# Kernel tuning notes

Measured on AMD Instinct MI355X. Metric: run time of the kernel, lower is better.

Reference implementation:

```python
import jax, jax.numpy as jnp
import numpy as np

N_NODES = 100000
N_EDGES = 1600000


def _degree_norms(src, dst, n):
    ones = jnp.ones(src.shape[0], dtype=jnp.float32)
    deg_out = jax.ops.segment_sum(ones, src, num_segments=n)
    deg_in = jax.ops.segment_sum(ones, dst, num_segments=n)
    src_norm = jax.lax.rsqrt(jnp.maximum(deg_out, 1.0))
    dst_norm = jax.lax.rsqrt(jnp.maximum(deg_in, 1.0))
    return src_norm, dst_norm


def _graph_conv(x, W, b, src, dst, src_norm, dst_norm, n):
    # DGL GraphConv, norm='both': D_dst^{-1/2} A D_src^{-1/2} X W + b
    # Apply W first (same math, smaller messages).
    h = x @ W                                  # [N, out]
    m = (h * src_norm[:, None])[src]           # [E, out] gather
    agg = jax.ops.segment_sum(m, dst, num_segments=n)  # [N, out] scatter-add
    return agg * dst_norm[:, None] + b


def setup_inputs() -> dict:
    key = jax.random.key(0)
    ks = jax.random.split(key, 10)
    inp = {
        "x": jax.random.normal(ks[0], (N_NODES, 128), dtype=jnp.float32),
        "src": jax.random.randint(ks[1], (N_EDGES,), 0, N_NODES, dtype=jnp.int32),
        "dst": jax.random.randint(ks[2], (N_EDGES,), 0, N_NODES, dtype=jnp.int32),
        "W1": jax.random.normal(ks[3], (128, 64), dtype=jnp.float32) * 0.08,
        "b1": jnp.zeros((64,), dtype=jnp.float32),
        "W2": jax.random.normal(ks[4], (64, 64), dtype=jnp.float32) * 0.12,
        "b2": jnp.zeros((64,), dtype=jnp.float32),
        "W3": jax.random.normal(ks[5], (64, 64), dtype=jnp.float32) * 0.12,
        "b3": jnp.zeros((64,), dtype=jnp.float32),
        "W4": jax.random.normal(ks[6], (64, 64), dtype=jnp.float32) * 0.12,
        "b4": jnp.zeros((64,), dtype=jnp.float32),
        "Wres": jax.random.normal(ks[7], (128, 64), dtype=jnp.float32) * 0.08,
        "bres": jnp.zeros((64,), dtype=jnp.float32),
        "Wop": jax.random.normal(ks[8], (64, 16), dtype=jnp.float32) * 0.12,
        "bop": jnp.zeros((16,), dtype=jnp.float32),
    }
    return inp


def reference(x, src, dst, W1, b1, W2, b2, W3, b3, W4, b4, Wres, bres, Wop, bop):
    n = x.shape[0]
    src_norm, dst_norm = _degree_norms(src, dst, n)
    res = x @ Wres + bres
    out = jax.nn.relu(_graph_conv(x, W1, b1, src, dst, src_norm, dst_norm, n))
    out = jax.nn.relu(_graph_conv(out, W2, b2, src, dst, src_norm, dst_norm, n))
    out = jax.nn.relu(_graph_conv(out, W3, b3, src, dst, src_norm, dst_norm, n))
    out = _graph_conv(out, W4, b4, src, dst, src_norm, dst_norm, n)
    out = jax.nn.relu(out + res)
    return out @ Wop + bop
```

## Files before the change

### kernel.cpp

```cpp
#include <hip/hip_runtime.h>
#include <cstdint>
#include <cstddef>


#define SLOTS 64
#define BCAP 5120
#define ACHUNK 4096

__device__ __forceinline__ unsigned short f2bf(float f) {
  union { float f; unsigned u; } v; v.f = f;
  unsigned r = (v.u + 0x7fffu + ((v.u >> 16) & 1u)) >> 16;
  return (unsigned short)r;
}
__device__ __forceinline__ float bf2f(unsigned short h) {
  union { unsigned u; float f; } v; v.u = ((unsigned)h) << 16;
  return v.f;
}
__device__ __forceinline__ void bf2x2(unsigned u, float* lo, float* hi) {
  union { unsigned x; float f; } a, b;
  a.x = u << 16; b.x = u & 0xFFFF0000u;
  *lo = a.f; *hi = b.f;
}

__global__ void init_kernel(int* __restrict__ gcur_d, int* __restrict__ gcur_s, int nbuck) {
  int i = blockIdx.x * blockDim.x + threadIdx.x;
  if (i < nbuck) { gcur_d[i] = 0; gcur_s[i] = 0; }
}

__global__ __launch_bounds__(256) void bucket_kernel(
    const int* __restrict__ src, const int* __restrict__ dst,
    int* __restrict__ gcur_d, int* __restrict__ gcur_s,
    unsigned* __restrict__ dbuck, unsigned char* __restrict__ sbuck,
    int E, int nbuck) {
  __shared__ int s_src[ACHUNK];
  __shared__ int s_dst[ACHUNK];
  __shared__ int run_d[512];
  __shared__ int run_s[512];
  const int t = threadIdx.x;
  const int base = blockIdx.x * ACHUNK;
  int cnt = E - base;
  if (cnt > ACHUNK) cnt = ACHUNK;

  for (int i = t; i < cnt; i += 256) {
    s_src[i] = src[base + i];
    s_dst[i] = dst[base + i];
  }
  for (int i = t; i < nbuck; i += 256) { run_d[i] = 0; run_s[i] = 0; }
  __syncthreads();
  for (int i = t; i < cnt; i += 256) {
    atomicAdd(&run_d[s_dst[i] >> 8], 1);
    atomicAdd(&run_s[s_src[i] >> 8], 1);
  }
  __syncthreads();
  {
    const int iters = (nbuck + 255) >> 8;
    for (int it = 0; it < iters; ++it) {
      int i = it * 256 + t;
      int hd = 0, hs = 0;
      if (i < nbuck) { hd = run_d[i]; hs = run_s[i]; }
      __syncthreads();
      if (i < nbuck) {
        run_d[i] = hd ? atomicAdd(&gcur_d[i], hd) : 0;
        run_s[i] = hs ? atomicAdd(&gcur_s[i], hs) : 0;
      }
      __syncthreads();
    }
  }
  for (int i = t; i < cnt; i += 256) {
    int d = s_dst[i], s = s_src[i];
    int bd = d >> 8;
    int pd = atomicAdd(&run_d[bd], 1);
    if (pd < BCAP) dbuck[(size_t)bd * BCAP + pd] = ((unsigned)(d & 255) << 24) | (unsigned)s;
    int bs = s >> 8;
    int ps = atomicAdd(&run_s[bs], 1);
    if (ps < BCAP) sbuck[(size_t)bs * BCAP + ps] = (unsigned char)(s & 255);
  }
}

__global__ __launch_bounds__(256) void csr_kernel(
    const unsigned* __restrict__ dbuck, const int* __restrict__ gcur_d,
    int* __restrict__ col, int* __restrict__ cnt_arr,
    float* __restrict__ dnorm, int N) {
  __shared__ int cur[256];
  const int b = blockIdx.x;
  const int t = threadIdx.x;
  const int node0 = b << 8;
  cur[t] = 0;
  __syncthreads();
  int cnt = gcur_d[b];
  if (cnt > BCAP) cnt = BCAP;
  const unsigned* p = dbuck + (size_t)b * BCAP;
  for (int i = t; i < cnt; i += 256) {
    unsigned e = p[i];
    int nl = e >> 24;
    int s = (int)(e & 0x00FFFFFFu);
    int pos = atomicAdd(&cur[nl], 1);
    if (pos < SLOTS) col[(size_t)(node0 + nl) * SLOTS + pos] = s;
  }
  __syncthreads();
  int node = node0 + t;
  if (node < N) {
    int c = cur[t];
    cnt_arr[node] = c;
    float d = (float)(c < 1 ? 1 : c);
    dnorm[node] = rsqrtf(d);
  }
}

__global__ __launch_bounds__(256) void degout_kernel(
    const unsigned char* __restrict__ sbuck, const int* __restrict__ gcur_s,
    float* __restrict__ snorm, int N) {
  __shared__ int cur[256];
  const int b = blockIdx.x;
  const int t = threadIdx.x;
  cur[t] = 0;
  __syncthreads();
  int cnt = gcur_s[b];
  if (cnt > BCAP) cnt = BCAP;
  const unsigned char* p = sbuck + (size_t)b * BCAP;
  for (int i = t; i < cnt; i += 256) atomicAdd(&cur[p[i]], 1);
  __syncthreads();
  int node = (b << 8) + t;
  if (node < N) {
    int c = cur[t];
    snorm[node] = rsqrtf((float)(c < 1 ? 1 : c));
  }
}

#define GEMM_STEP(ACC, r, aval, wv)                 \
  ACC[r][0] = fmaf((aval), (wv).x, ACC[r][0]);      \
  ACC[r][1] = fmaf((aval), (wv).y, ACC[r][1]);      \
  ACC[r][2] = fmaf((aval), (wv).z, ACC[r][2]);      \
  ACC[r][3] = fmaf((aval), (wv).w, ACC[r][3]);

#define GEMM_ROW(ACC, W_LDS, kc)                                         \
  { float4 w0 = *(const float4*)&W_LDS[kc + 0][tx4];                     \
    float4 w1 = *(const float4*)&W_LDS[kc + 1][tx4];                     \
    float4 w2 = *(const float4*)&W_LDS[kc + 2][tx4];                     \
    float4 w3 = *(const float4*)&W_LDS[kc + 3][tx4];                     \
    GEMM_STEP(ACC, 0, a0.x, w0) GEMM_STEP(ACC, 0, a0.y, w1) GEMM_STEP(ACC, 0, a0.z, w2) GEMM_STEP(ACC, 0, a0.w, w3) \
    GEMM_STEP(ACC, 1, a1.x, w0) GEMM_STEP(ACC, 1, a1.y, w1) GEMM_STEP(ACC, 1, a1.z, w2) GEMM_STEP(ACC, 1, a1.w, w3) \
    GEMM_STEP(ACC, 2, a2.x, w0) GEMM_STEP(ACC, 2, a2.y, w1) GEMM_STEP(ACC, 2, a2.z, w2) GEMM_STEP(ACC, 2, a2.w, w3) \
    GEMM_STEP(ACC, 3, a3.x, w0) GEMM_STEP(ACC, 3, a3.y, w1) GEMM_STEP(ACC, 3, a3.z, w2) GEMM_STEP(ACC, 3, a3.w, w3) }

#define STAGE_W_TILE(W_PTR, W_LDS)                                \
  { const float* s_ = (W_PTR) + (size_t)srow * 64 + scol;         \
    float4 q0 = *(const float4*)(s_ + 0);                         \
    float4 q1 = *(const float4*)(s_ + 4);                         \
    float4 q2 = *(const float4*)(s_ + 8);                         \
    float4 q3 = *(const float4*)(s_ + 12);                        \
    *(float4*)&W_LDS[srow][scol + 0]  = q0;                       \
    *(float4*)&W_LDS[srow][scol + 4]  = q1;                       \
    *(float4*)&W_LDS[srow][scol + 8]  = q2;                       \
    *(float4*)&W_LDS[srow][scol + 12] = q3; }

__global__ __launch_bounds__(256) void gemm1_kernel(
    const float* __restrict__ X, const float* __restrict__ W1,
    const float* __restrict__ Wres, const float* __restrict__ bres,
    const float* __restrict__ norm,
    unsigned short* __restrict__ Hout, unsigned short* __restrict__ Rout, int n) {
  __shared__ float in_lds[64][68];
  __shared__ float w_lds[64][64];
  __shared__ float wr_lds[64][64];
  const int t = threadIdx.x;
  const int tx4 = (t & 15) * 4;
  const int ty4 = (t >> 4) * 4;
  const int node0 = blockIdx.x * 64;
  const int srow = t >> 2;
  const int scol = (t & 3) * 16;

  float acc[4][4], acc2[4][4];
#pragma unroll
  for (int r = 0; r < 4; r++)
#pragma unroll
    for (int j = 0; j < 4; j++) { acc[r][j] = 0.f; acc2[r][j] = 0.f; }

  for (int kb = 0; kb < 128; kb += 64) {
    {
      int gi = node0 + srow;
      float4 v0, v1, v2, v3;
      if (gi < n) {
        const float* s = X + (size_t)gi * 128 + kb + scol;
        v0 = *(const float4*)(s + 0);
        v1 = *(const float4*)(s + 4);
        v2 = *(const float4*)(s + 8);
        v3 = *(const float4*)(s + 12);
      } else {
        v0 = v1 = v2 = v3 = make_float4(0.f, 0.f, 0.f, 0.f);
      }
      *(float4*)&in_lds[srow][scol + 0]  = v0;
      *(float4*)&in_lds[srow][scol + 4]  = v1;
      *(float4*)&in_lds[srow][scol + 8]  = v2;
      *(float4*)&in_lds[srow][scol + 12] = v3;
    }
    STAGE_W_TILE(W1 + (size_t)kb * 64, w_lds)
    STAGE_W_TILE(Wres + (size_t)kb * 64, wr_lds)
    __syncthreads();

    for (int kc = 0; kc < 64; kc += 4) {
      float4 a0 = *(const float4*)&in_lds[ty4 + 0][kc];
      float4 a1 = *(const float4*)&in_lds[ty4 + 1][kc];
      float4 a2 = *(const float4*)&in_lds[ty4 + 2][kc];
      float4 a3 = *(const float4*)&in_lds[ty4 + 3][kc];
      GEMM_ROW(acc, w_lds, kc)
      GEMM_ROW(acc2, wr_lds, kc)
    }
    __syncthreads();
  }

#pragma unroll
  for (int r = 0; r < 4; r++) {
    int gi = node0 + ty4 + r;
    if (gi >= n) continue;
    float s = norm[gi];
    ushort4 h;
    h.x = f2bf(acc[r][0] * s);
    h.y = f2bf(acc[r][1] * s);
    h.z = f2bf(acc[r][2] * s);
    h.w = f2bf(acc[r][3] * s);
    *(ushort4*)&Hout[(size_t)gi * 64 + tx4] = h;
    ushort4 rr;
    rr.x = f2bf(acc2[r][0] + bres[tx4 + 0]);
    rr.y = f2bf(acc2[r][1] + bres[tx4 + 1]);
    rr.z = f2bf(acc2[r][2] + bres[tx4 + 2]);
    rr.w = f2bf(acc2[r][3] + bres[tx4 + 3]);
    *(ushort4*)&Rout[(size_t)gi * 64 + tx4] = rr;
  }
}

__global__ __launch_bounds__(256) void gemm_bf16_kernel(
    const unsigned short* __restrict__ X, const float* __restrict__ W,
    const float* __restrict__ norm, unsigned short* __restrict__ out, int n) {
  __shared__ float in_lds[64][68];
  __shared__ float w_lds[64][64];
  const int t = threadIdx.x;
  const int tx4 = (t & 15) * 4;
  const int ty4 = (t >> 4) * 4;
  const int node0 = blockIdx.x * 64;
  const int srow = t >> 2;
  const int scol = (t & 3) * 16;

  float acc[4][4];
#pragma unroll
  for (int r = 0; r < 4; r++)
#pragma unroll
    for (int j = 0; j < 4; j++) acc[r][j] = 0.f;

  {
    int gi = node0 + srow;
    float f[16];
    if (gi < n) {
      const unsigned short* s = X + (size_t)gi * 64 + scol;
      uint4 u0 = *(const uint4*)(s + 0);
      uint4 u1 = *(const uint4*)(s + 8);
      bf2x2(u0.x, &f[0], &f[1]);   bf2x2(u0.y, &f[2], &f[3]);
      bf2x2(u0.z, &f[4], &f[5]);   bf2x2(u0.w, &f[6], &f[7]);
      bf2x2(u1.x, &f[8], &f[9]);   bf2x2(u1.y, &f[10], &f[11]);
      bf2x2(u1.z, &f[12], &f[13]); bf2x2(u1.w, &f[14], &f[15]);
    } else {
#pragma unroll
      for (int j = 0; j < 16; j++) f[j] = 0.f;
    }
#pragma unroll
    for (int j = 0; j < 16; j += 4)
      *(float4*)&in_lds[srow][scol + j] = make_float4(f[j], f[j+1], f[j+2], f[j+3]);
  }
  STAGE_W_TILE(W, w_lds)
  __syncthreads();

  for (int kc = 0; kc < 64; kc += 4) {
    float4 a0 = *(const float4*)&in_lds[ty4 + 0][kc];
    float4 a1 = *(const float4*)&in_lds[ty4 + 1][kc];
    float4 a2 = *(const float4*)&in_lds[ty4 + 2][kc];
    float4 a3 = *(const float4*)&in_lds[ty4 + 3][kc];
    GEMM_ROW(acc, w_lds, kc)
  }

#pragma unroll
  for (int r = 0; r < 4; r++) {
    int gi = node0 + ty4 + r;
    if (gi >= n) continue;
    float s = norm[gi];
    ushort4 o;
    o.x = f2bf(acc[r][0] * s);
    o.y = f2bf(acc[r][1] * s);
    o.z = f2bf(acc[r][2] * s);
    o.w = f2bf(acc[r][3] * s);
    *(ushort4*)&out[(size_t)gi * 64 + tx4] = o;
  }
}

#define UNPACK_ADD(u, A)                         \
  { float f0, f1, f2, f3;                        \
    bf2x2((u).x, &f0, &f1);                      \
    bf2x2((u).y, &f2, &f3);                      \
    A[0] += f0; A[1] += f1; A[2] += f2; A[3] += f3; }

template <int RELU>
__global__ __launch_bounds__(256) void agg_kernel(
    const unsigned short* __restrict__ H, const int* __restrict__ cnt_arr,
    const int* __restrict__ col, const float* __restrict__ dnorm,
    const float* __restrict__ bias, unsigned short* __restrict__ O,
    int n) {
  const int lane = threadIdx.x & 63;
  const int sub = lane >> 4;
  const int fl  = lane & 15;
  const int wave = (blockIdx.x * blockDim.x + threadIdx.x) >> 6;
  const int nwaves = (gridDim.x * blockDim.x) >> 6;
  const uint2* __restrict__ H2 = (const uint2*)H;
  const float4 bb = ((const float4*)bias)[fl];

  for (int v0 = wave * 2; v0 < n; v0 += nwaves * 2) {
    const int v1 = v0 + 1;
    int cnt0 = cnt_arr[v0];
    int cnt1 = (v1 < n) ? cnt_arr[v1] : 0;
    if (cnt0 > SLOTS) cnt0 = SLOTS;
    if (cnt1 > SLOTS) cnt1 = SLOTS;
    const size_t base0 = (size_t)v0 * SLOTS;
    const size_t base1 = (size_t)v1 * SLOTS;
    int cv0 = (lane < cnt0) ? col[base0 + lane] : 0;
    int cv1 = (lane < cnt1) ? col[base1 + lane] : 0;
    float a0[4] = {0.f, 0.f, 0.f, 0.f};
    float b0[4] = {0.f, 0.f, 0.f, 0.f};
    float a1[4] = {0.f, 0.f, 0.f, 0.f};
    float b1[4] = {0.f, 0.f, 0.f, 0.f};
    const int cmax = cnt0 > cnt1 ? cnt0 : cnt1;
    for (int j = 0; j < cmax; j += 8) {
      const int e0 = j + sub;
      const int e1 = j + 4 + sub;
      int c00 = __shfl(cv0, e0);
      int c01 = __shfl(cv0, e1);
      int c10 = __shfl(cv1, e0);
      int c11 = __shfl(cv1, e1);
      if (e0 < cnt0) { uint2 u = H2[(size_t)c00 * 16 + fl]; UNPACK_ADD(u, a0) }
      if (e0 < cnt1) { uint2 u = H2[(size_t)c10 * 16 + fl]; UNPACK_ADD(u, a1) }
      if (e1 < cnt0) { uint2 u = H2[(size_t)c01 * 16 + fl]; UNPACK_ADD(u, b0) }
      if (e1 < cnt1) { uint2 u = H2[(size_t)c11 * 16 + fl]; UNPACK_ADD(u, b1) }
    }
    float r0[4], r1[4];
#pragma unroll
    for (int i = 0; i < 4; i++) {
      float s0 = a0[i] + b0[i];
      s0 += __shfl_xor(s0, 16);
      s0 += __shfl_xor(s0, 32);
      r0[i] = s0;
      float s1 = a1[i] + b1[i];
      s1 += __shfl_xor(s1, 16);
      s1 += __shfl_xor(s1, 32);
      r1[i] = s1;
    }
    if (sub == 0) {
      float d = dnorm[v0];
      float q0 = r0[0] * d + bb.x;
      float q1 = r0[1] * d + bb.y;
      float q2 = r0[2] * d + bb.z;
      float q3 = r0[3] * d + bb.w;
      if (RELU) {
        q0 = fmaxf(q0, 0.f); q1 = fmaxf(q1, 0.f);
        q2 = fmaxf(q2, 0.f); q3 = fmaxf(q3, 0.f);
      }
      ushort4 o;
      o.x = f2bf(q0); o.y = f2bf(q1); o.z = f2bf(q2); o.w = f2bf(q3);
      *(ushort4*)&O[base0 + 4 * fl] = o;
    } else if (sub == 1 && v1 < n) {
      float d = dnorm[v1];
      float q0 = r1[0] * d + bb.x;
      float q1 = r1[1] * d + bb.y;
      float q2 = r1[2] * d + bb.z;
      float q3 = r1[3] * d + bb.w;
      if (RELU) {
        q0 = fmaxf(q0, 0.f); q1 = fmaxf(q1, 0.f);
        q2 = fmaxf(q2, 0.f); q3 = fmaxf(q3, 0.f);
      }
      ushort4 o;
      o.x = f2bf(q0); o.y = f2bf(q1); o.z = f2bf(q2); o.w = f2bf(q3);
      *(ushort4*)&O[base1 + 4 * fl] = o;
    }
  }
}

__global__ __launch_bounds__(256) void final_kernel(
    const unsigned short* __restrict__ O4, const unsigned short* __restrict__ R,
    const float* __restrict__ Wop, const float* __restrict__ bop,
    float* __restrict__ out, int n) {
  __shared__ float t_lds[64][68];
  __shared__ float wop_lds[64][16];
  const int t = threadIdx.x;
  const int node0 = blockIdx.x * 64;
  const int srow = t >> 2;
  const int scol = (t & 3) * 16;

  ((float4*)&wop_lds[0][0])[t] = ((const float4*)Wop)[t];

  {
    int gi = node0 + srow;
    float f[16];
    if (gi < n) {
      const unsigned short* po = O4 + (size_t)gi * 64 + scol;
      const unsigned short* pr = R + (size_t)gi * 64 + scol;
      uint4 uo0 = *(const uint4*)(po + 0);
      uint4 uo1 = *(const uint4*)(po + 8);
      uint4 ur0 = *(const uint4*)(pr + 0);
      uint4 ur1 = *(const uint4*)(pr + 8);
      float o0, o1, rr0, rr1;
#define ADDRELU2(UO, UR, idx)                         \
      bf2x2(UO, &o0, &o1); bf2x2(UR, &rr0, &rr1);     \
      f[idx] = fmaxf(o0 + rr0, 0.f);                  \
      f[idx + 1] = fmaxf(o1 + rr1, 0.f);
      ADDRELU2(uo0.x, ur0.x, 0)  ADDRELU2(uo0.y, ur0.y, 2)
      ADDRELU2(uo0.z, ur0.z, 4)  ADDRELU2(uo0.w, ur0.w, 6)
      ADDRELU2(uo1.x, ur1.x, 8)  ADDRELU2(uo1.y, ur1.y, 10)
      ADDRELU2(uo1.z, ur1.z, 12) ADDRELU2(uo1.w, ur1.w, 14)
#undef ADDRELU2
    } else {
#pragma unroll
      for (int j = 0; j < 16; j++) f[j] = 0.f;
    }
#pragma unroll
    for (int j = 0; j < 16; j += 4)
      *(float4*)&t_lds[srow][scol + j] = make_float4(f[j], f[j+1], f[j+2], f[j+3]);
  }
  __syncthreads();

  {
    int nn = t >> 2;
    int fg = t & 3;
    float4 a = ((const float4*)bop)[fg];
#pragma unroll 16
    for (int k = 0; k < 64; k++) {
      float tv = t_lds[nn][k];
      float4 w = *(const float4*)&wop_lds[k][fg * 4];
      a.x = fmaf(tv, w.x, a.x);
      a.y = fmaf(tv, w.y, a.y);
      a.z = fmaf(tv, w.z, a.z);
      a.w = fmaf(tv, w.w, a.w);
    }
    int node = node0 + nn;
    if (node < n) *(float4*)&out[(size_t)node * 16 + fg * 4] = a;
  }
}

extern "C" void kernel_launch(void* const* d_in, const int* in_sizes, int n_in,
                              void* d_out, int out_size, void* d_ws, size_t ws_size,
                              hipStream_t stream) {
  const float* x    = (const float*)d_in[0];
  const int*   src  = (const int*)d_in[1];
  const int*   dst  = (const int*)d_in[2];
  const float* W1   = (const float*)d_in[3];
  const float* b1   = (const float*)d_in[4];
  const float* W2   = (const float*)d_in[5];
  const float* b2   = (const float*)d_in[6];
  const float* W3   = (const float*)d_in[7];
  const float* b3   = (const float*)d_in[8];
  const float* W4   = (const float*)d_in[9];
  const float* b4   = (const float*)d_in[10];
  const float* Wres = (const float*)d_in[11];
  const float* bres = (const float*)d_in[12];
  const float* Wop  = (const float*)d_in[13];
  const float* bop  = (const float*)d_in[14];
  float* out = (float*)d_out;

  const int N = in_sizes[0] / 128;
  const int E = in_sizes[1];
  const int nbuck = (N + 255) >> 8;

  char* p = (char*)d_ws;
  auto alloc = [&](size_t b) {
    char* r = p;
    p += (b + 255) & ~(size_t)255;
    return r;
  };
  int*            gcur_d  = (int*)alloc((size_t)nbuck * 4);
  int*            gcur_s  = (int*)alloc((size_t)nbuck * 4);
  unsigned*       dbuck   = (unsigned*)alloc((size_t)nbuck * BCAP * 4);
  unsigned char*  sbuck   = (unsigned char*)alloc((size_t)nbuck * BCAP);
  int*            col     = (int*)alloc((size_t)N * SLOTS * 4);
  int*            cnt_arr = (int*)alloc((size_t)N * 4);
  float*          snorm   = (float*)alloc((size_t)N * 4);
  float*          dnorm   = (float*)alloc((size_t)N * 4);
  unsigned short* Hbuf    = (unsigned short*)alloc((size_t)N * 64 * 2);
  unsigned short* Obuf    = (unsigned short*)alloc((size_t)N * 64 * 2);
  unsigned short* Rbuf    = (unsigned short*)alloc((size_t)N * 64 * 2);

  init_kernel<<<(nbuck + 255) / 256, 256, 0, stream>>>(gcur_d, gcur_s, nbuck);

  int ga = (E + ACHUNK - 1) / ACHUNK;
  bucket_kernel<<<ga, 256, 0, stream>>>(src, dst, gcur_d, gcur_s, dbuck, sbuck, E, nbuck);
  csr_kernel<<<nbuck, 256, 0, stream>>>(dbuck, gcur_d, col, cnt_arr, dnorm, N);
  degout_kernel<<<nbuck, 256, 0, stream>>>(sbuck, gcur_s, snorm, N);

  int gb = (N + 63) / 64;
  gemm1_kernel<<<gb, 256, 0, stream>>>(x, W1, Wres, bres, snorm, Hbuf, Rbuf, N);
  agg_kernel<1><<<2048, 256, 0, stream>>>(Hbuf, cnt_arr, col, dnorm, b1, Obuf, N);
  gemm_bf16_kernel<<<gb, 256, 0, stream>>>(Obuf, W2, snorm, Hbuf, N);
  agg_kernel<1><<<2048, 256, 0, stream>>>(Hbuf, cnt_arr, col, dnorm, b2, Obuf, N);
  gemm_bf16_kernel<<<gb, 256, 0, stream>>>(Obuf, W3, snorm, Hbuf, N);
  agg_kernel<1><<<2048, 256, 0, stream>>>(Hbuf, cnt_arr, col, dnorm, b3, Obuf, N);
  gemm_bf16_kernel<<<gb, 256, 0, stream>>>(Obuf, W4, snorm, Hbuf, N);
  agg_kernel<0><<<2048, 256, 0, stream>>>(Hbuf, cnt_arr, col, dnorm, b4, Obuf, N);
  final_kernel<<<gb, 256, 0, stream>>>(Obuf, Rbuf, Wop, bop, out, N);
}
```

Before: 326.5 us.

## Use bf16 MFMA for dense layers and unroll aggregation gathers

Replaces the scalar FMA GEMM kernels with MFMA 16x16x32 bf16 kernels. The weights are transposed and converted to bf16 in a prep kernel that also zeroes the bucket counters, and the first layer's input is converted to bf16 on load. The aggregation kernel now reads column indices straight from global memory instead of shuffling them across lanes, and issues 16 edges per iteration to raise memory-level parallelism. The first layer loses some precision because its input and weights become bf16, and the aggregation makes more global index loads.

```diff
diff --git a/kernel.cpp b/kernel.cpp
--- a/kernel.cpp
+++ b/kernel.cpp
@@ -6,6 +6,9 @@
 #define SLOTS 64
 #define BCAP 5120
 #define ACHUNK 4096
+
+typedef __attribute__((ext_vector_type(8))) short bf16x8;
+typedef __attribute__((ext_vector_type(4))) float f32x4;
 
 __device__ __forceinline__ unsigned short f2bf(float f) {
   union { float f; unsigned u; } v; v.f = f;
@@ -22,9 +25,29 @@
   *lo = a.f; *hi = b.f;
 }
 
-__global__ void init_kernel(int* __restrict__ gcur_d, int* __restrict__ gcur_s, int nbuck) {
+__global__ void prep_kernel(const float* __restrict__ W1, const float* __restrict__ W2,
+                            const float* __restrict__ W3, const float* __restrict__ W4,
+                            const float* __restrict__ Wres,
+                            unsigned short* __restrict__ WT,
+                            int* __restrict__ gcur_d, int* __restrict__ gcur_s, int nbuck) {
   int i = blockIdx.x * blockDim.x + threadIdx.x;
   if (i < nbuck) { gcur_d[i] = 0; gcur_s[i] = 0; }
+  if (i < 8192) {
+    int c = i >> 7, k = i & 127;
+    WT[i] = f2bf(W1[k * 64 + c]);
+  } else if (i < 12288) {
+    int j = i - 8192; int c = j >> 6, k = j & 63;
+    WT[i] = f2bf(W2[k * 64 + c]);
+  } else if (i < 16384) {
+    int j = i - 12288; int c = j >> 6, k = j & 63;
+    WT[i] = f2bf(W3[k * 64 + c]);
+  } else if (i < 20480) {
+    int j = i - 16384; int c = j >> 6, k = j & 63;
+    WT[i] = f2bf(W4[k * 64 + c]);
+  } else if (i < 28672) {
+    int j = i - 20480; int c = j >> 7, k = j & 127;
+    WT[i] = f2bf(Wres[k * 64 + c]);
+  }
 }
 
 __global__ __launch_bounds__(256) void bucket_kernel(
@@ -127,166 +150,152 @@
   }
 }
 
-#define GEMM_STEP(ACC, r, aval, wv)                 \
-  ACC[r][0] = fmaf((aval), (wv).x, ACC[r][0]);      \
-  ACC[r][1] = fmaf((aval), (wv).y, ACC[r][1]);      \
-  ACC[r][2] = fmaf((aval), (wv).z, ACC[r][2]);      \
-  ACC[r][3] = fmaf((aval), (wv).w, ACC[r][3]);
-
-#define GEMM_ROW(ACC, W_LDS, kc)                                         \
-  { float4 w0 = *(const float4*)&W_LDS[kc + 0][tx4];                     \
-    float4 w1 = *(const float4*)&W_LDS[kc + 1][tx4];                     \
-    float4 w2 = *(const float4*)&W_LDS[kc + 2][tx4];                     \
-    float4 w3 = *(const float4*)&W_LDS[kc + 3][tx4];                     \
-    GEMM_STEP(ACC, 0, a0.x, w0) GEMM_STEP(ACC, 0, a0.y, w1) GEMM_STEP(ACC, 0, a0.z, w2) GEMM_STEP(ACC, 0, a0.w, w3) \
-    GEMM_STEP(ACC, 1, a1.x, w0) GEMM_STEP(ACC, 1, a1.y, w1) GEMM_STEP(ACC, 1, a1.z, w2) GEMM_STEP(ACC, 1, a1.w, w3) \
-    GEMM_STEP(ACC, 2, a2.x, w0) GEMM_STEP(ACC, 2, a2.y, w1) GEMM_STEP(ACC, 2, a2.z, w2) GEMM_STEP(ACC, 2, a2.w, w3) \
-    GEMM_STEP(ACC, 3, a3.x, w0) GEMM_STEP(ACC, 3, a3.y, w1) GEMM_STEP(ACC, 3, a3.z, w2) GEMM_STEP(ACC, 3, a3.w, w3) }
-
-#define STAGE_W_TILE(W_PTR, W_LDS)                                \
-  { const float* s_ = (W_PTR) + (size_t)srow * 64 + scol;         \
-    float4 q0 = *(const float4*)(s_ + 0);                         \
-    float4 q1 = *(const float4*)(s_ + 4);                         \
-    float4 q2 = *(const float4*)(s_ + 8);                         \
-    float4 q3 = *(const float4*)(s_ + 12);                        \
-    *(float4*)&W_LDS[srow][scol + 0]  = q0;                       \
-    *(float4*)&W_LDS[srow][scol + 4]  = q1;                       \
-    *(float4*)&W_LDS[srow][scol + 8]  = q2;                       \
-    *(float4*)&W_LDS[srow][scol + 12] = q3; }
-
-__global__ __launch_bounds__(256) void gemm1_kernel(
-    const float* __restrict__ X, const float* __restrict__ W1,
-    const float* __restrict__ Wres, const float* __restrict__ bres,
+__global__ __launch_bounds__(256) void gemm_mfma_kernel(
+    const unsigned short* __restrict__ X, const unsigned short* __restrict__ WT,
+    const float* __restrict__ norm, unsigned short* __restrict__ out, int n) {
+  __shared__ float ol[64][68];
+  const int t = threadIdx.x;
+  const int l = t & 63;
+  const int w = t >> 6;
+  const int node0 = blockIdx.x * 64;
+  const int row = l & 15, kg = l >> 4;
+
+  int arow = node0 + w * 16 + row;
+  if (arow > n - 1) arow = n - 1;
+  const unsigned short* ab = X + (size_t)arow * 64 + kg * 8;
+  bf16x8 a0 = *(const bf16x8*)(ab);
+  bf16x8 a1 = *(const bf16x8*)(ab + 32);
+
+  f32x4 acc[4];
+#pragma unroll
+  for (int ct = 0; ct < 4; ct++) acc[ct] = (f32x4){0.f, 0.f, 0.f, 0.f};
+
+#pragma unroll
+  for (int ct = 0; ct < 4; ct++) {
+    const unsigned short* wb = WT + (size_t)(ct * 16 + row) * 64 + kg * 8;
+    bf16x8 b0 = *(const bf16x8*)(wb);
+    bf16x8 b1 = *(const bf16x8*)(wb + 32);
+    acc[ct] = __builtin_amdgcn_mfma_f32_16x16x32_bf16(a0, b0, acc[ct], 0, 0, 0);
+    acc[ct] = __builtin_amdgcn_mfma_f32_16x16x32_bf16(a1, b1, acc[ct], 0, 0, 0);
+  }
+
+#pragma unroll
+  for (int ct = 0; ct < 4; ct++)
+#pragma unroll
+    for (int i = 0; i < 4; i++)
+      ol[w * 16 + kg * 4 + i][ct * 16 + row] = acc[ct][i];
+  __syncthreads();
+
+  {
+    int r2 = t >> 2, cg = (t & 3) * 16;
+    int node = node0 + r2;
+    if (node < n) {
+      float s = norm[node];
+      unsigned short o[16];
+#pragma unroll
+      for (int i = 0; i < 16; i++) o[i] = f2bf(ol[r2][cg + i] * s);
+      *(uint4*)&out[(size_t)node * 64 + cg] = *(const uint4*)&o[0];
+      *(uint4*)&out[(size_t)node * 64 + cg + 8] = *(const uint4*)&o[8];
+    }
+  }
+}
+
+__global__ __launch_bounds__(256) void gemm1_mfma_kernel(
+    const float* __restrict__ X, const unsigned short* __restrict__ W1T,
+    const unsigned short* __restrict__ WresT, const float* __restrict__ bres,
     const float* __restrict__ norm,
     unsigned short* __restrict__ Hout, unsigned short* __restrict__ Rout, int n) {
-  __shared__ float in_lds[64][68];
-  __shared__ float w_lds[64][64];
-  __shared__ float wr_lds[64][64];
+  __shared__ unsigned short in_bf[64][136];
+  __shared__ float ol[64][68];
   const int t = threadIdx.x;
-  const int tx4 = (t & 15) * 4;
-  const int ty4 = (t >> 4) * 4;
+  const int l = t & 63;
+  const int w = t >> 6;
   const int node0 = blockIdx.x * 64;
-  const int srow = t >> 2;
-  const int scol = (t & 3) * 16;
-
-  float acc[4][4], acc2[4][4];
-#pragma unroll
-  for (int r = 0; r < 4; r++)
-#pragma unroll
-    for (int j = 0; j < 4; j++) { acc[r][j] = 0.f; acc2[r][j] = 0.f; }
-
-  for (int kb = 0; kb < 128; kb += 64) {
-    {
-      int gi = node0 + srow;
-      float4 v0, v1, v2, v3;
-      if (gi < n) {
-        const float* s = X + (size_t)gi * 128 + kb + scol;
-        v0 = *(const float4*)(s + 0);
-        v1 = *(const float4*)(s + 4);
-        v2 = *(const float4*)(s + 8);
-        v3 = *(const float4*)(s + 12);
-      } else {
-        v0 = v1 = v2 = v3 = make_float4(0.f, 0.f, 0.f, 0.f);
+  const int row = l & 15, kg = l >> 4;
+
+  {
+    int r = t >> 2, cb = (t & 3) * 32;
+    int gi = node0 + r;
+    unsigned short tmp[32];
+    if (gi < n) {
+      const float* s = X + (size_t)gi * 128 + cb;
+#pragma unroll
+      for (int q = 0; q < 32; q += 4) {
+        float4 f = *(const float4*)(s + q);
+        tmp[q] = f2bf(f.x); tmp[q + 1] = f2bf(f.y);
+        tmp[q + 2] = f2bf(f.z); tmp[q + 3] = f2bf(f.w);
       }
-      *(float4*)&in_lds[srow][scol + 0]  = v0;
-      *(float4*)&in_lds[srow][scol + 4]  = v1;
-      *(float4*)&in_lds[srow][scol + 8]  = v2;
-      *(float4*)&in_lds[srow][scol + 12] = v3;
-    }
-    STAGE_W_TILE(W1 + (size_t)kb * 64, w_lds)
-    STAGE_W_TILE(Wres + (size_t)kb * 64, wr_lds)
-    __syncthreads();
-
-    for (int kc = 0; kc < 64; kc += 4) {
-      float4 a0 = *(const float4*)&in_lds[ty4 + 0][kc];
-      float4 a1 = *(const float4*)&in_lds[ty4 + 1][kc];
-      float4 a2 = *(const float4*)&in_lds[ty4 + 2][kc];
-      float4 a3 = *(const float4*)&in_lds[ty4 + 3][kc];
-      GEMM_ROW(acc, w_lds, kc)
-      GEMM_ROW(acc2, wr_lds, kc)
-    }
-    __syncthreads();
-  }
-
-#pragma unroll
-  for (int r = 0; r < 4; r++) {
-    int gi = node0 + ty4 + r;
-    if (gi >= n) continue;
-    float s = norm[gi];
-    ushort4 h;
-    h.x = f2bf(acc[r][0] * s);
-    h.y = f2bf(acc[r][1] * s);
-    h.z = f2bf(acc[r][2] * s);
-    h.w = f2bf(acc[r][3] * s);
-    *(ushort4*)&Hout[(size_t)gi * 64 + tx4] = h;
-    ushort4 rr;
-    rr.x = f2bf(acc2[r][0] + bres[tx4 + 0]);
-    rr.y = f2bf(acc2[r][1] + bres[tx4 + 1]);
-    rr.z = f2bf(acc2[r][2] + bres[tx4 + 2]);
-    rr.w = f2bf(acc2[r][3] + bres[tx4 + 3]);
-    *(ushort4*)&Rout[(size_t)gi * 64 + tx4] = rr;
-  }
-}
-
-__global__ __launch_bounds__(256) void gemm_bf16_kernel(
-    const unsigned short* __restrict__ X, const float* __restrict__ W,
-    const float* __restrict__ norm, unsigned short* __restrict__ out, int n) {
-  __shared__ float in_lds[64][68];
-  __shared__ float w_lds[64][64];
-  const int t = threadIdx.x;
-  const int tx4 = (t & 15) * 4;
-  const int ty4 = (t >> 4) * 4;
-  const int node0 = blockIdx.x * 64;
-  const int srow = t >> 2;
-  const int scol = (t & 3) * 16;
-
-  float acc[4][4];
-#pragma unroll
-  for (int r = 0; r < 4; r++)
-#pragma unroll
-    for (int j = 0; j < 4; j++) acc[r][j] = 0.f;
-
-  {
-    int gi = node0 + srow;
-    float f[16];
-    if (gi < n) {
-      const unsigned short* s = X + (size_t)gi * 64 + scol;
-      uint4 u0 = *(const uint4*)(s + 0);
-      uint4 u1 = *(const uint4*)(s + 8);
-      bf2x2(u0.x, &f[0], &f[1]);   bf2x2(u0.y, &f[2], &f[3]);
-      bf2x2(u0.z, &f[4], &f[5]);   bf2x2(u0.w, &f[6], &f[7]);
-      bf2x2(u1.x, &f[8], &f[9]);   bf2x2(u1.y, &f[10], &f[11]);
-      bf2x2(u1.z, &f[12], &f[13]); bf2x2(u1.w, &f[14], &f[15]);
     } else {
 #pragma unroll
-      for (int j = 0; j < 16; j++) f[j] = 0.f;
-    }
-#pragma unroll
-    for (int j = 0; j < 16; j += 4)
-      *(float4*)&in_lds[srow][scol + j] = make_float4(f[j], f[j+1], f[j+2], f[j+3]);
-  }
-  STAGE_W_TILE(W, w_lds)
-  __syncthreads();
-
-  for (int kc = 0; kc < 64; kc += 4) {
-    float4 a0 = *(const float4*)&in_lds[ty4 + 0][kc];
-    float4 a1 = *(const float4*)&in_lds[ty4 + 1][kc];
-    float4 a2 = *(const float4*)&in_lds[ty4 + 2][kc];
-    float4 a3 = *(const float4*)&in_lds[ty4 + 3][kc];
-    GEMM_ROW(acc, w_lds, kc)
-  }
-
-#pragma unroll
-  for (int r = 0; r < 4; r++) {
-    int gi = node0 + ty4 + r;
-    if (gi >= n) continue;
-    float s = norm[gi];
-    ushort4 o;
-    o.x = f2bf(acc[r][0] * s);
-    o.y = f2bf(acc[r][1] * s);
-    o.z = f2bf(acc[r][2] * s);
-    o.w = f2bf(acc[r][3] * s);
-    *(ushort4*)&out[(size_t)gi * 64 + tx4] = o;
+      for (int q = 0; q < 32; q++) tmp[q] = 0;
+    }
+#pragma unroll
+    for (int q = 0; q < 32; q += 8)
+      *(uint4*)&in_bf[r][cb + q] = *(const uint4*)&tmp[q];
+  }
+  __syncthreads();
+
+  bf16x8 a[4];
+#pragma unroll
+  for (int kh = 0; kh < 4; kh++)
+    a[kh] = *(const bf16x8*)&in_bf[w * 16 + row][kh * 32 + kg * 8];
+
+  f32x4 acc[4], acc2[4];
+#pragma unroll
+  for (int ct = 0; ct < 4; ct++) {
+    acc[ct] = (f32x4){0.f, 0.f, 0.f, 0.f};
+    acc2[ct] = (f32x4){0.f, 0.f, 0.f, 0.f};
+  }
+
+#pragma unroll
+  for (int kh = 0; kh < 4; kh++) {
+#pragma unroll
+    for (int ct = 0; ct < 4; ct++) {
+      const unsigned short* wb1 = W1T + (size_t)(ct * 16 + row) * 128 + kh * 32 + kg * 8;
+      const unsigned short* wbr = WresT + (size_t)(ct * 16 + row) * 128 + kh * 32 + kg * 8;
+      bf16x8 b1 = *(const bf16x8*)(wb1);
+      bf16x8 br = *(const bf16x8*)(wbr);
+      acc[ct] = __builtin_amdgcn_mfma_f32_16x16x32_bf16(a[kh], b1, acc[ct], 0, 0, 0);
+      acc2[ct] = __builtin_amdgcn_mfma_f32_16x16x32_bf16(a[kh], br, acc2[ct], 0, 0, 0);
+    }
+  }
+
+#pragma unroll
+  for (int ct = 0; ct < 4; ct++)
+#pragma unroll
+    for (int i = 0; i < 4; i++)
+      ol[w * 16 + kg * 4 + i][ct * 16 + row] = acc[ct][i];
+  __syncthreads();
+  {
+    int r2 = t >> 2, cg = (t & 3) * 16;
+    int node = node0 + r2;
+    if (node < n) {
+      float s = norm[node];
+      unsigned short o[16];
+#pragma unroll
+      for (int i = 0; i < 16; i++) o[i] = f2bf(ol[r2][cg + i] * s);
+      *(uint4*)&Hout[(size_t)node * 64 + cg] = *(const uint4*)&o[0];
+      *(uint4*)&Hout[(size_t)node * 64 + cg + 8] = *(const uint4*)&o[8];
+    }
+  }
+  __syncthreads();
+
+#pragma unroll
+  for (int ct = 0; ct < 4; ct++)
+#pragma unroll
+    for (int i = 0; i < 4; i++)
+      ol[w * 16 + kg * 4 + i][ct * 16 + row] = acc2[ct][i];
+  __syncthreads();
+  {
+    int r2 = t >> 2, cg = (t & 3) * 16;
+    int node = node0 + r2;
+    if (node < n) {
+      unsigned short o[16];
+#pragma unroll
+      for (int i = 0; i < 16; i++) o[i] = f2bf(ol[r2][cg + i] + bres[cg + i]);
+      *(uint4*)&Rout[(size_t)node * 64 + cg] = *(const uint4*)&o[0];
+      *(uint4*)&Rout[(size_t)node * 64 + cg + 8] = *(const uint4*)&o[8];
+    }
   }
 }
 
@@ -303,8 +312,8 @@
     const float* __restrict__ bias, unsigned short* __restrict__ O,
     int n) {
   const int lane = threadIdx.x & 63;
-  const int sub = lane >> 4;
-  const int fl  = lane & 15;
+  const int g = lane >> 4;
+  const int fl = lane & 15;
   const int wave = (blockIdx.x * blockDim.x + threadIdx.x) >> 6;
   const int nwaves = (gridDim.x * blockDim.x) >> 6;
   const uint2* __restrict__ H2 = (const uint2*)H;
@@ -316,26 +325,28 @@
     int cnt1 = (v1 < n) ? cnt_arr[v1] : 0;
     if (cnt0 > SLOTS) cnt0 = SLOTS;
     if (cnt1 > SLOTS) cnt1 = SLOTS;
-    const size_t base0 = (size_t)v0 * SLOTS;
-    const size_t base1 = (size_t)v1 * SLOTS;
-    int cv0 = (lane < cnt0) ? col[base0 + lane] : 0;
-    int cv1 = (lane < cnt1) ? col[base1 + lane] : 0;
+    const int* cp0 = col + (size_t)v0 * SLOTS;
+    const int* cp1 = (v1 < n) ? col + (size_t)v1 * SLOTS : cp0;
     float a0[4] = {0.f, 0.f, 0.f, 0.f};
     float b0[4] = {0.f, 0.f, 0.f, 0.f};
     float a1[4] = {0.f, 0.f, 0.f, 0.f};
     float b1[4] = {0.f, 0.f, 0.f, 0.f};
     const int cmax = cnt0 > cnt1 ? cnt0 : cnt1;
-    for (int j = 0; j < cmax; j += 8) {
-      const int e0 = j + sub;
-      const int e1 = j + 4 + sub;
-      int c00 = __shfl(cv0, e0);
-      int c01 = __shfl(cv0, e1);
-      int c10 = __shfl(cv1, e0);
-      int c11 = __shfl(cv1, e1);
+    for (int j = 0; j < cmax; j += 16) {
+      const int e0 = j + g;
+      const int e1 = j + 4 + g;
+      const int e2 = j + 8 + g;
+      const int e3 = j + 12 + g;
+      int c00 = cp0[e0], c01 = cp0[e1], c02 = cp0[e2], c03 = cp0[e3];
+      int c10 = cp1[e0], c11 = cp1[e1], c12 = cp1[e2], c13 = cp1[e3];
       if (e0 < cnt0) { uint2 u = H2[(size_t)c00 * 16 + fl]; UNPACK_ADD(u, a0) }
+      if (e1 < cnt0) { uint2 u = H2[(size_t)c01 * 16 + fl]; UNPACK_ADD(u, b0) }
+      if (e2 < cnt0) { uint2 u = H2[(size_t)c02 * 16 + fl]; UNPACK_ADD(u, a0) }
+      if (e3 < cnt0) { uint2 u = H2[(size_t)c03 * 16 + fl]; UNPACK_ADD(u, b0) }
       if (e0 < cnt1) { uint2 u = H2[(size_t)c10 * 16 + fl]; UNPACK_ADD(u, a1) }
-      if (e1 < cnt0) { uint2 u = H2[(size_t)c01 * 16 + fl]; UNPACK_ADD(u, b0) }
       if (e1 < cnt1) { uint2 u = H2[(size_t)c11 * 16 + fl]; UNPACK_ADD(u, b1) }
+      if (e2 < cnt1) { uint2 u = H2[(size_t)c12 * 16 + fl]; UNPACK_ADD(u, a1) }
+      if (e3 < cnt1) { uint2 u = H2[(size_t)c13 * 16 + fl]; UNPACK_ADD(u, b1) }
     }
     float r0[4], r1[4];
 #pragma unroll
@@ -349,7 +360,7 @@
       s1 += __shfl_xor(s1, 32);
       r1[i] = s1;
     }
-    if (sub == 0) {
+    if (g == 0) {
       float d = dnorm[v0];
       float q0 = r0[0] * d + bb.x;
       float q1 = r0[1] * d + bb.y;
@@ -361,8 +372,8 @@
       }
       ushort4 o;
       o.x = f2bf(q0); o.y = f2bf(q1); o.z = f2bf(q2); o.w = f2bf(q3);
-      *(ushort4*)&O[base0 + 4 * fl] = o;
-    } else if (sub == 1 && v1 < n) {
+      *(ushort4*)&O[(size_t)v0 * SLOTS + 4 * fl] = o;
+    } else if (g == 1 && v1 < n) {
       float d = dnorm[v1];
       float q0 = r1[0] * d + bb.x;
       float q1 = r1[1] * d + bb.y;
@@ -374,7 +385,7 @@
       }
       ushort4 o;
       o.x = f2bf(q0); o.y = f2bf(q1); o.z = f2bf(q2); o.w = f2bf(q3);
-      *(ushort4*)&O[base1 + 4 * fl] = o;
+      *(ushort4*)&O[(size_t)v1 * SLOTS + 4 * fl] = o;
     }
   }
 }
@@ -472,6 +483,7 @@
   };
   int*            gcur_d  = (int*)alloc((size_t)nbuck * 4);
   int*            gcur_s  = (int*)alloc((size_t)nbuck * 4);
+  unsigned short* WT      = (unsigned short*)alloc(28672 * 2);
   unsigned*       dbuck   = (unsigned*)alloc((size_t)nbuck * BCAP * 4);
   unsigned char*  sbuck   = (unsigned char*)alloc((size_t)nbuck * BCAP);
   int*            col     = (int*)alloc((size_t)N * SLOTS * 4);
@@ -482,7 +494,13 @@
   unsigned short* Obuf    = (unsigned short*)alloc((size_t)N * 64 * 2);
   unsigned short* Rbuf    = (unsigned short*)alloc((size_t)N * 64 * 2);
 
-  init_kernel<<<(nbuck + 255) / 256, 256, 0, stream>>>(gcur_d, gcur_s, nbuck);
+  unsigned short* W1T   = WT;
+  unsigned short* W2T   = WT + 8192;
+  unsigned short* W3T   = WT + 12288;
+  unsigned short* W4T   = WT + 16384;
+  unsigned short* WresT = WT + 20480;
+
+  prep_kernel<<<112, 256, 0, stream>>>(W1, W2, W3, W4, Wres, WT, gcur_d, gcur_s, nbuck);
 
   int ga = (E + ACHUNK - 1) / ACHUNK;
   bucket_kernel<<<ga, 256, 0, stream>>>(src, dst, gcur_d, gcur_s, dbuck, sbuck, E, nbuck);
@@ -490,13 +508,13 @@
   degout_kernel<<<nbuck, 256, 0, stream>>>(sbuck, gcur_s, snorm, N);
 
   int gb = (N + 63) / 64;
-  gemm1_kernel<<<gb, 256, 0, stream>>>(x, W1, Wres, bres, snorm, Hbuf, Rbuf, N);
+  gemm1_mfma_kernel<<<gb, 256, 0, stream>>>(x, W1T, WresT, bres, snorm, Hbuf, Rbuf, N);
   agg_kernel<1><<<2048, 256, 0, stream>>>(Hbuf, cnt_arr, col, dnorm, b1, Obuf, N);
-  gemm_bf16_kernel<<<gb, 256, 0, stream>>>(Obuf, W2, snorm, Hbuf, N);
+  gemm_mfma_kernel<<<gb, 256, 0, stream>>>(Obuf, W2T, snorm, Hbuf, N);
   agg_kernel<1><<<2048, 256, 0, stream>>>(Hbuf, cnt_arr, col, dnorm, b2, Obuf, N);
-  gemm_bf16_kernel<<<gb, 256, 0, stream>>>(Obuf, W3, snorm, Hbuf, N);
+  gemm_mfma_kernel<<<gb, 256, 0, stream>>>(Obuf, W3T, snorm, Hbuf, N);
   agg_kernel<1><<<2048, 256, 0, stream>>>(Hbuf, cnt_arr, col, dnorm, b3, Obuf, N);
-  gemm_bf16_kernel<<<gb, 256, 0, stream>>>(Obuf, W4, snorm, Hbuf, N);
+  gemm_mfma_kernel<<<gb, 256, 0, stream>>>(Obuf, W4T, snorm, Hbuf, N);
   agg_kernel<0><<<2048, 256, 0, stream>>>(Hbuf, cnt_arr, col, dnorm, b4, Obuf, N);
   final_kernel<<<gb, 256, 0, stream>>>(Obuf, Rbuf, Wop, bop, out, N);
 }
```

New measurement: 326.7 us. About the same (+0.1%).
